# Kernel optimization log

Measured on AMD Instinct MI355X. Metric: run time of the kernel, lower is better.

The kernel has to match this reference:

```python
import jax, jax.numpy as jnp
import numpy as np

EMBED = 768
HEADS = 12
HDIM = EMBED // HEADS
FF = EMBED * 2
B, LQ, LK = 4, 2048, 2048


def _linear(x, W, b):
    # W: [in, out]
    return x @ W + b


def _layernorm(x, g, b, eps=1e-5):
    mu = jnp.mean(x, axis=-1, keepdims=True)
    var = jnp.mean(jnp.square(x - mu), axis=-1, keepdims=True)
    return (x - mu) * jax.lax.rsqrt(var + eps) * g + b


def _l2norm(x, eps=1e-12):
    # matches F.normalize: x / max(||x||_2, eps)
    n = jnp.sqrt(jnp.sum(jnp.square(x), axis=-1, keepdims=True))
    return x / jnp.maximum(n, eps)


def _heads(x):
    b, l, _ = x.shape
    return x.reshape(b, l, HEADS, HDIM).transpose(0, 2, 1, 3)  # [B,H,L,hd]


def setup_inputs() -> dict:
    key = jax.random.key(0)
    ks = jax.random.split(key, 20)
    s = 0.02
    d = {
        'image_tokens': jax.random.normal(ks[0], (B, LQ, EMBED), jnp.float32),
        'point_tokens': jax.random.normal(ks[1], (B, LK, EMBED), jnp.float32),
        'image_pos': jax.random.normal(ks[2], (B, LQ, EMBED), jnp.float32),
        'point_pos': jax.random.normal(ks[3], (B, LK, EMBED), jnp.float32),
        'Wip': jax.random.normal(ks[4], (EMBED, EMBED), jnp.float32) * s,
        'bip': jnp.zeros((EMBED,), jnp.float32),
        'Wpp': jax.random.normal(ks[5], (EMBED, EMBED), jnp.float32) * s,
        'bpp': jnp.zeros((EMBED,), jnp.float32),
        'Wq': jax.random.normal(ks[6], (EMBED, EMBED), jnp.float32) * s,
        'bq': jnp.zeros((EMBED,), jnp.float32),
        'Wk': jax.random.normal(ks[7], (EMBED, EMBED), jnp.float32) * s,
        'bk': jnp.zeros((EMBED,), jnp.float32),
        'Wv': jax.random.normal(ks[8], (EMBED, EMBED), jnp.float32) * s,
        'bv': jnp.zeros((EMBED,), jnp.float32),
        'Wo': jax.random.normal(ks[9], (EMBED, EMBED), jnp.float32) * s,
        'bo': jnp.zeros((EMBED,), jnp.float32),
        'g1': jnp.ones((EMBED,), jnp.float32),
        'b1': jnp.zeros((EMBED,), jnp.float32),
        'g2': jnp.ones((EMBED,), jnp.float32),
        'b2': jnp.zeros((EMBED,), jnp.float32),
        'Wf1': jax.random.normal(ks[10], (EMBED, FF), jnp.float32) * s,
        'bf1': jnp.zeros((FF,), jnp.float32),
        'Wf2': jax.random.normal(ks[11], (FF, EMBED), jnp.float32) * s,
        'bf2': jnp.zeros((EMBED,), jnp.float32),
    }
    return d


def reference(image_tokens, point_tokens, image_pos, point_pos,
              Wip, bip, Wpp, bpp, Wq, bq, Wk, bk, Wv, bv, Wo, bo,
              g1, b1, g2, b2, Wf1, bf1, Wf2, bf2):
    q = _linear(image_tokens + _linear(image_pos, Wip, bip), Wq, bq)
    k = _linear(point_tokens + _linear(point_pos, Wpp, bpp), Wk, bk)
    v = _linear(point_tokens, Wv, bv)

    q = _l2norm(_heads(q))  # [B,H,Lq,hd]
    k = _l2norm(_heads(k))  # [B,H,Lk,hd]
    v = _heads(v)           # [B,H,Lk,hd]

    scores = jnp.einsum('bhqd,bhkd->bhqk', q, k)
    attn = jax.nn.softmax(scores, axis=-1)
    fused = jnp.einsum('bhqk,bhkd->bhqd', attn, v)
    fused = fused.transpose(0, 2, 1, 3).reshape(image_tokens.shape[0], image_tokens.shape[1], EMBED)

    fused = _layernorm(image_tokens + _linear(fused, Wo, bo), g1, b1)
    h = _linear(fused, Wf1, bf1)
    h = 0.5 * h * (1.0 + jax.lax.erf(h / jnp.sqrt(jnp.float32(2.0))))  # exact GELU
    ff = _linear(h, Wf2, bf2)
    return _layernorm(fused + ff, g2, b2)
```

## Files before the change

kernel.cpp:

```cpp
#include <hip/hip_runtime.h>

#define EMBED 768
#define FFDIM 1536
#define BATCH 4
#define SEQ   2048
#define HEADS 12
#define MROWS (BATCH*SEQ)

typedef __attribute__((ext_vector_type(4)))  float  f32x4;
typedef __attribute__((ext_vector_type(16))) float  f32x16;
typedef __attribute__((ext_vector_type(8)))  __bf16 bf16x8;
typedef __attribute__((ext_vector_type(4)))  short  s16x4;

__device__ __forceinline__ short f2bf(float f) {
    union { float f; unsigned u; } x; x.f = f;
    unsigned r = x.u + 0x7fffu + ((x.u >> 16) & 1u);
    return (short)(r >> 16);
}

__device__ __forceinline__ unsigned cvtpk(float lo, float hi) {
    unsigned r;
    asm("v_cvt_pk_bf16_f32 %0, %1, %2" : "=v"(r) : "v"(lo), "v"(hi));
    return r;
}

__device__ __forceinline__ void gll16(const void* g, void* l) {
    __builtin_amdgcn_global_load_lds(
        (const __attribute__((address_space(1))) void*)g,
        (__attribute__((address_space(3))) void*)l, 16, 0, 0);
}

__device__ __forceinline__ bf16x8 ldsw(const short* base, int row, int chunk) {
    return *(const bf16x8*)((const char*)base + row * 128 + (((chunk ^ (row & 7))) << 4));
}

__global__ __launch_bounds__(256) void cvt3_kernel(
    const float* __restrict__ s0, const float* __restrict__ s1,
    const float* __restrict__ s2,
    short* __restrict__ o0, short* __restrict__ o1, short* __restrict__ o2)
{
    const float* s; short* o;
    switch (blockIdx.y) {
        case 0:  s = s0; o = o0; break;
        case 1:  s = s1; o = o1; break;
        default: s = s2; o = o2; break;
    }
    size_t i = ((size_t)blockIdx.x * 256 + threadIdx.x) * 4;
    float4 v = *(const float4*)(s + i);
    s16x4 r;
    r[0] = f2bf(v.x); r[1] = f2bf(v.y); r[2] = f2bf(v.z); r[3] = f2bf(v.w);
    *(s16x4*)(o + i) = r;
}

__global__ __launch_bounds__(256) void transpose_w(
    const float* __restrict__ W, short* __restrict__ Wt, int K, int N)
{
    __shared__ float tile[32][33];
    const int k0 = blockIdx.y * 32, n0 = blockIdx.x * 32;
    const int tx = threadIdx.x & 31, ty = threadIdx.x >> 5;
    #pragma unroll
    for (int i = 0; i < 32; i += 8)
        tile[ty + i][tx] = W[(size_t)(k0 + ty + i) * N + n0 + tx];
    __syncthreads();
    #pragma unroll
    for (int i = 0; i < 32; i += 8)
        Wt[(size_t)(n0 + ty + i) * K + k0 + tx] = f2bf(tile[tx][ty + i]);
}

__global__ __launch_bounds__(256) void transpose_v(
    const short* __restrict__ v, short* __restrict__ vt)
{
    __shared__ short tile[64][65];
    const int bh = blockIdx.y;
    const int b = bh / HEADS, h = bh % HEADS;
    const int k0 = blockIdx.x * 64;
    const int tx = threadIdx.x & 63, ty = threadIdx.x >> 6;
    #pragma unroll
    for (int i = 0; i < 64; i += 4)
        tile[ty + i][tx] = v[(size_t)(b * SEQ + k0 + ty + i) * EMBED + h * 64 + tx];
    __syncthreads();
    #pragma unroll
    for (int i = 0; i < 64; i += 4)
        vt[(size_t)(bh * 64 + ty + i) * SEQ + k0 + tx] = tile[tx][ty + i];
}

template<int L2N, int GELU_, int SBF, int SF32>
__device__ __forceinline__ void gemm_core(
    const short* __restrict__ A, const short* __restrict__ Wt,
    const float* __restrict__ bias, const float* __restrict__ resid,
    short* __restrict__ outb, float* __restrict__ outf, int N, int K)
{
    __shared__ short As[2][128][32];
    __shared__ short Bs[2][128][32];
    const int tid = threadIdx.x;
    const int mbase = blockIdx.y * 128, nbase = blockIdx.x * 128;
    const int wid = tid >> 6, lane = tid & 63;
    const int wm = wid >> 1, wn = wid & 1;
    const int l15 = lane & 15, lhi = lane >> 4;
    const int sr = tid >> 2;
    const int sc = (tid & 3) * 8;

    f32x4 acc[4][4] = {};

    const short* Ab = A  + (size_t)mbase * K;
    const short* Bb = Wt + (size_t)nbase * K;

#define GSTAGE(buf, kk)                                                         \
    gll16(Ab + (size_t)sr * K        + (kk) + sc, &As[buf][sr][sc]);            \
    gll16(Ab + (size_t)(64 + sr) * K + (kk) + sc, &As[buf][64 + sr][sc]);       \
    gll16(Bb + (size_t)sr * K        + (kk) + sc, &Bs[buf][sr][sc]);            \
    gll16(Bb + (size_t)(64 + sr) * K + (kk) + sc, &Bs[buf][64 + sr][sc]);

    GSTAGE(0, 0);
    __syncthreads();

    const int nk = K >> 5;
    for (int t = 0; t < nk; ++t) {
        const int cur = t & 1;
        if (t + 1 < nk) { GSTAGE(cur ^ 1, (t + 1) << 5); }
        bf16x8 av[4], bv[4];
        #pragma unroll
        for (int tt = 0; tt < 4; ++tt) {
            av[tt] = *(const bf16x8*)(&As[cur][wm * 64 + tt * 16 + l15][lhi * 8]);
            bv[tt] = *(const bf16x8*)(&Bs[cur][wn * 64 + tt * 16 + l15][lhi * 8]);
        }
        #pragma unroll
        for (int mt = 0; mt < 4; ++mt)
            #pragma unroll
            for (int nt = 0; nt < 4; ++nt)
                acc[mt][nt] = __builtin_amdgcn_mfma_f32_16x16x32_bf16(
                    av[mt], bv[nt], acc[mt][nt], 0, 0, 0);
        __syncthreads();
    }
#undef GSTAGE

    #pragma unroll
    for (int mt = 0; mt < 4; ++mt) {
        float vals[4][4];
        #pragma unroll
        for (int nt = 0; nt < 4; ++nt) {
            const int col = nbase + wn * 64 + nt * 16 + l15;
            const float bc = bias[col];
            #pragma unroll
            for (int j = 0; j < 4; ++j) vals[nt][j] = acc[mt][nt][j] + bc;
        }
        if (resid != nullptr) {
            #pragma unroll
            for (int nt = 0; nt < 4; ++nt) {
                const int col = nbase + wn * 64 + nt * 16 + l15;
                #pragma unroll
                for (int j = 0; j < 4; ++j) {
                    const int row = mbase + wm * 64 + mt * 16 + lhi * 4 + j;
                    vals[nt][j] += resid[(size_t)row * N + col];
                }
            }
        }
        if (L2N) {
            #pragma unroll
            for (int j = 0; j < 4; ++j) {
                float s = 0.f;
                #pragma unroll
                for (int nt = 0; nt < 4; ++nt) s += vals[nt][j] * vals[nt][j];
                s += __shfl_xor(s, 1); s += __shfl_xor(s, 2);
                s += __shfl_xor(s, 4); s += __shfl_xor(s, 8);
                const float inv = 1.0f / fmaxf(sqrtf(s), 1e-12f);
                #pragma unroll
                for (int nt = 0; nt < 4; ++nt) vals[nt][j] *= inv;
            }
        }
        if (GELU_) {
            #pragma unroll
            for (int nt = 0; nt < 4; ++nt)
                #pragma unroll
                for (int j = 0; j < 4; ++j) {
                    const float v = vals[nt][j];
                    vals[nt][j] = 0.5f * v * (1.0f + erff(v * 0.70710678118654752f));
                }
        }
        #pragma unroll
        for (int nt = 0; nt < 4; ++nt) {
            const int col = nbase + wn * 64 + nt * 16 + l15;
            #pragma unroll
            for (int j = 0; j < 4; ++j) {
                const int row = mbase + wm * 64 + mt * 16 + lhi * 4 + j;
                if (SBF)  outb[(size_t)row * N + col] = f2bf(vals[nt][j]);
                if (SF32) outf[(size_t)row * N + col] = vals[nt][j];
            }
        }
    }
}

template<int L2N, int GELU_, int SBF, int SF32>
__global__ __launch_bounds__(256) void gemm_bt(
    const short* __restrict__ A, const short* __restrict__ Wt,
    const float* __restrict__ bias, const float* __restrict__ resid,
    short* __restrict__ outb, float* __restrict__ outf, int N, int K)
{
    gemm_core<L2N, GELU_, SBF, SF32>(A, Wt, bias, resid, outb, outf, N, K);
}

__global__ __launch_bounds__(256) void gemm3_kernel(
    const short* A0, const short* W0, const float* b0, const float* r0, short* o0,
    const short* A1, const short* W1, const float* b1, const float* r1, short* o1,
    const short* A2, const short* W2, const float* b2, const float* r2, short* o2)
{
    const short *A, *W; const float *bi, *re; short* ob;
    if (blockIdx.z == 0)      { A = A0; W = W0; bi = b0; re = r0; ob = o0; }
    else if (blockIdx.z == 1) { A = A1; W = W1; bi = b1; re = r1; ob = o1; }
    else                      { A = A2; W = W2; bi = b2; re = r2; ob = o2; }
    gemm_core<0, 0, 1, 0>(A, W, bi, re, ob, nullptr, EMBED, EMBED);
}

__global__ __launch_bounds__(256) void gemm2_kernel(
    const short* A0, const short* W0, const float* b0, short* o0,
    const short* A1, const short* W1, const float* b1, short* o1)
{
    const short *A, *W; const float *bi; short* ob;
    if (blockIdx.z == 0) { A = A0; W = W0; bi = b0; ob = o0; }
    else                 { A = A1; W = W1; bi = b1; ob = o1; }
    gemm_core<1, 0, 1, 0>(A, W, bi, nullptr, ob, nullptr, EMBED, EMBED);
}

__global__ __launch_bounds__(256) void attn_kernel(
    const short* __restrict__ qn, const short* __restrict__ kn,
    const short* __restrict__ vt, short* __restrict__ outp)
{
    __shared__ short Ks[2][64][64];
    __shared__ short Vs[2][64][64];

    const int bh = blockIdx.y;
    const int b = bh / HEADS, h = bh % HEADS;
    const int q0 = blockIdx.x * 128;
    const int tid = threadIdx.x, wq = tid >> 6, lane = tid & 63;
    const int l31 = lane & 31, hi = lane >> 5;
    const int srow = tid >> 3;
    const int schk = tid & 7;

    const size_t qrow = (size_t)(b * SEQ + q0 + wq * 32 + l31) * EMBED + h * 64;
    bf16x8 qf[4];
    #pragma unroll
    for (int t = 0; t < 4; ++t)
        qf[t] = *(const bf16x8*)(qn + qrow + t * 16 + hi * 8);

    const short* kbase = kn + (size_t)b * SEQ * EMBED + h * 64;
    const short* vbase = vt + (size_t)bh * 64 * SEQ;

#define ASTAGE(buf, k0x) do {                                                            \
    _Pragma("unroll")                                                                    \
    for (int rr = 0; rr < 2; ++rr) {                                                     \
        const int row = rr * 32 + srow;                                                  \
        gll16(kbase + (size_t)((k0x) + row) * EMBED + ((schk ^ (row & 7)) * 8),          \
              &Ks[buf][row][schk * 8]);                                                  \
        gll16(vbase + (size_t)row * SEQ + (k0x) + ((schk ^ (row & 7)) * 8),              \
              &Vs[buf][row][schk * 8]);                                                  \
    }                                                                                    \
} while (0)

    ASTAGE(0, 0);
    __syncthreads();

    f32x16 acc_o[2] = {};
    float rsum = 0.f;
    const int NT = SEQ / 64;

    for (int kt = 0; kt < NT; ++kt) {
        const int cur = kt & 1;
        if (kt + 1 < NT) { ASTAGE(cur ^ 1, (kt + 1) * 64); }

        f32x16 s0 = {}, s1 = {};
        #pragma unroll
        for (int t = 0; t < 4; ++t) {
            bf16x8 kf0 = ldsw(&Ks[cur][0][0], l31,      t * 2 + hi);
            bf16x8 kf1 = ldsw(&Ks[cur][0][0], 32 + l31, t * 2 + hi);
            s0 = __builtin_amdgcn_mfma_f32_32x32x16_bf16(kf0, qf[t], s0, 0, 0, 0);
            s1 = __builtin_amdgcn_mfma_f32_32x32x16_bf16(kf1, qf[t], s1, 0, 0, 0);
        }

        float e0[16], e1[16];
        #pragma unroll
        for (int i = 0; i < 16; ++i) { const float e = __expf(s0[i]); rsum += e; e0[i] = e; }
        #pragma unroll
        for (int i = 0; i < 16; ++i) { const float e = __expf(s1[i]); rsum += e; e1[i] = e; }

        unsigned w[2][8], sw[2][8];
        #pragma unroll
        for (int a = 0; a < 4; ++a) {
            w[0][2*a]   = cvtpk(e0[4*a],   e0[4*a+1]);
            w[0][2*a+1] = cvtpk(e0[4*a+2], e0[4*a+3]);
            w[1][2*a]   = cvtpk(e1[4*a],   e1[4*a+1]);
            w[1][2*a+1] = cvtpk(e1[4*a+2], e1[4*a+3]);
        }
        #pragma unroll
        for (int kb = 0; kb < 2; ++kb)
            #pragma unroll
            for (int i = 0; i < 8; ++i)
                sw[kb][i] = (unsigned)__shfl_xor((int)w[kb][i], 32);

        #pragma unroll
        for (int kb = 0; kb < 2; ++kb) {
            #pragma unroll
            for (int ks = 0; ks < 2; ++ks) {
                union { unsigned u[4]; bf16x8 v; } pf;
                pf.u[0] = hi ? sw[kb][4*ks+2] : w[kb][4*ks];
                pf.u[1] = hi ? sw[kb][4*ks+3] : w[kb][4*ks+1];
                pf.u[2] = hi ? w[kb][4*ks+2]  : sw[kb][4*ks];
                pf.u[3] = hi ? w[kb][4*ks+3]  : sw[kb][4*ks+1];
                #pragma unroll
                for (int db = 0; db < 2; ++db) {
                    bf16x8 vf = ldsw(&Vs[cur][0][0], db * 32 + l31, kb * 4 + ks * 2 + hi);
                    acc_o[db] = __builtin_amdgcn_mfma_f32_32x32x16_bf16(vf, pf.v, acc_o[db], 0, 0, 0);
                }
            }
        }
        __syncthreads();
    }
#undef ASTAGE

    const float rtot = rsum + __shfl_xor(rsum, 32);
    const float rinv = 1.0f / rtot;

    short* Osb = &Ks[0][0][0];
    const int ql = wq * 32 + l31;
    #pragma unroll
    for (int db = 0; db < 2; ++db)
        #pragma unroll
        for (int a = 0; a < 4; ++a) {
            const float v0 = acc_o[db][4*a]   * rinv, v1 = acc_o[db][4*a+1] * rinv;
            const float v2 = acc_o[db][4*a+2] * rinv, v3 = acc_o[db][4*a+3] * rinv;
            uint2 pw; pw.x = cvtpk(v0, v1); pw.y = cvtpk(v2, v3);
            const int byteoff = ql * 128 + (((db * 4 + a) ^ (ql & 7)) << 4) + hi * 8;
            *(uint2*)((char*)Osb + byteoff) = pw;
        }
    __syncthreads();
    #pragma unroll
    for (int p = 0; p < 2; ++p) {
        const int r = p * 64 + (tid >> 2);
        #pragma unroll
        for (int i = 0; i < 2; ++i) {
            const int c = (tid & 3) * 2 + i;
            bf16x8 v = ldsw(Osb, r, c);
            *(bf16x8*)(outp + (size_t)(b * SEQ + q0 + r) * EMBED + h * 64 + c * 8) = v;
        }
    }
}

template<int SBF>
__global__ __launch_bounds__(256) void layernorm_768(
    const float* __restrict__ x, const float* __restrict__ g, const float* __restrict__ bb,
    float* __restrict__ outf, short* __restrict__ outb)
{
    const int row = blockIdx.x;
    const float* xr = x + (size_t)row * EMBED;
    const int t = threadIdx.x;
    const float v0 = xr[t], v1 = xr[t + 256], v2 = xr[t + 512];
    float s = v0 + v1 + v2;
    #pragma unroll
    for (int m = 1; m < 64; m <<= 1) s += __shfl_xor(s, m);
    __shared__ float red[4];
    __shared__ float red2[4];
    const int wid = t >> 6, lane = t & 63;
    if (lane == 0) red[wid] = s;
    __syncthreads();
    const float mu = (red[0] + red[1] + red[2] + red[3]) * (1.0f / 768.0f);
    const float d0 = v0 - mu, d1 = v1 - mu, d2 = v2 - mu;
    float ss = d0 * d0 + d1 * d1 + d2 * d2;
    #pragma unroll
    for (int m = 1; m < 64; m <<= 1) ss += __shfl_xor(ss, m);
    if (lane == 0) red2[wid] = ss;
    __syncthreads();
    const float var = (red2[0] + red2[1] + red2[2] + red2[3]) * (1.0f / 768.0f);
    const float inv = rsqrtf(var + 1e-5f);
    const float y0 = d0 * inv * g[t] + bb[t];
    const float y1 = d1 * inv * g[t + 256] + bb[t + 256];
    const float y2 = d2 * inv * g[t + 512] + bb[t + 512];
    float* of = outf + (size_t)row * EMBED;
    of[t] = y0; of[t + 256] = y1; of[t + 512] = y2;
    if (SBF) {
        short* ob = outb + (size_t)row * EMBED;
        ob[t] = f2bf(y0); ob[t + 256] = f2bf(y1); ob[t + 512] = f2bf(y2);
    }
}

extern "C" void kernel_launch(void* const* d_in, const int* in_sizes, int n_in,
                              void* d_out, int out_size, void* d_ws, size_t ws_size,
                              hipStream_t stream)
{
    (void)in_sizes; (void)n_in; (void)out_size; (void)ws_size;
    const float* itok = (const float*)d_in[0];
    const float* ptok = (const float*)d_in[1];
    const float* ipos = (const float*)d_in[2];
    const float* ppos = (const float*)d_in[3];
    const float* Wip = (const float*)d_in[4];  const float* bip = (const float*)d_in[5];
    const float* Wpp = (const float*)d_in[6];  const float* bpp = (const float*)d_in[7];
    const float* Wq  = (const float*)d_in[8];  const float* bq  = (const float*)d_in[9];
    const float* Wk  = (const float*)d_in[10]; const float* bk  = (const float*)d_in[11];
    const float* Wv  = (const float*)d_in[12]; const float* bv  = (const float*)d_in[13];
    const float* Wo  = (const float*)d_in[14]; const float* bo  = (const float*)d_in[15];
    const float* g1  = (const float*)d_in[16]; const float* b1  = (const float*)d_in[17];
    const float* g2  = (const float*)d_in[18]; const float* b2  = (const float*)d_in[19];
    const float* Wf1 = (const float*)d_in[20]; const float* bf1 = (const float*)d_in[21];
    const float* Wf2 = (const float*)d_in[22]; const float* bf2 = (const float*)d_in[23];
    float* out = (float*)d_out;

    char* ws = (char*)d_ws;
    constexpr size_t SZ_BF  = (size_t)MROWS * EMBED * 2;
    constexpr size_t SZ_F32 = (size_t)MROWS * EMBED * 4;
    constexpr size_t W768B  = (size_t)EMBED * EMBED * 2;
    constexpr size_t W1536B = (size_t)EMBED * FFDIM * 2;

    size_t o = 0;
    short* v_bf     = (short*)(ws + o); o += SZ_BF;
    short* pt_bf    = (short*)(ws + o); o += SZ_BF;
    short* ip_bf    = (short*)(ws + o); o += SZ_BF;
    short* pp_bf    = (short*)(ws + o); o += SZ_BF;
    short* qin_bf   = (short*)(ws + o); o += SZ_BF;
    short* kin_bf   = (short*)(ws + o); o += SZ_BF;
    short* qn_bf    = (short*)(ws + o); o += SZ_BF;
    short* kn_bf    = (short*)(ws + o); o += SZ_BF;
    short* attn_bf  = (short*)(ws + o); o += SZ_BF;
    float* x_f32    = (float*)(ws + o); o += SZ_F32;
    short* fused_bf = (short*)(ws + o); o += SZ_BF;
    float* fused_f32= (float*)(ws + o); o += SZ_F32;
    short* wip_t = (short*)(ws + o); o += W768B;
    short* wpp_t = (short*)(ws + o); o += W768B;
    short* wq_t  = (short*)(ws + o); o += W768B;
    short* wk_t  = (short*)(ws + o); o += W768B;
    short* wv_t  = (short*)(ws + o); o += W768B;
    short* wo_t  = (short*)(ws + o); o += W768B;
    short* wf1_t = (short*)(ws + o); o += W1536B;
    short* wf2_t = (short*)(ws + o); o += W1536B;
    short* vt_bf = pp_bf;
    short* h_bf  = qin_bf;

    const dim3 blk(256);

    cvt3_kernel<<<dim3(MROWS * EMBED / 1024, 3), blk, 0, stream>>>(
        ptok, ipos, ppos, pt_bf, ip_bf, pp_bf);

    transpose_w<<<dim3(EMBED / 32, EMBED / 32), blk, 0, stream>>>(Wip, wip_t, EMBED, EMBED);
    transpose_w<<<dim3(EMBED / 32, EMBED / 32), blk, 0, stream>>>(Wpp, wpp_t, EMBED, EMBED);
    transpose_w<<<dim3(EMBED / 32, EMBED / 32), blk, 0, stream>>>(Wq,  wq_t,  EMBED, EMBED);
    transpose_w<<<dim3(EMBED / 32, EMBED / 32), blk, 0, stream>>>(Wk,  wk_t,  EMBED, EMBED);
    transpose_w<<<dim3(EMBED / 32, EMBED / 32), blk, 0, stream>>>(Wv,  wv_t,  EMBED, EMBED);
    transpose_w<<<dim3(EMBED / 32, EMBED / 32), blk, 0, stream>>>(Wo,  wo_t,  EMBED, EMBED);
    transpose_w<<<dim3(FFDIM / 32, EMBED / 32), blk, 0, stream>>>(Wf1, wf1_t, EMBED, FFDIM);
    transpose_w<<<dim3(EMBED / 32, FFDIM / 32), blk, 0, stream>>>(Wf2, wf2_t, FFDIM, EMBED);

    gemm3_kernel<<<dim3(6, 64, 3), blk, 0, stream>>>(
        ip_bf, wip_t, bip, itok, qin_bf,
        pp_bf, wpp_t, bpp, ptok, kin_bf,
        pt_bf, wv_t,  bv,  nullptr, v_bf);

    gemm2_kernel<<<dim3(6, 64, 2), blk, 0, stream>>>(
        qin_bf, wq_t, bq, qn_bf,
        kin_bf, wk_t, bk, kn_bf);

    transpose_v<<<dim3(SEQ / 64, BATCH * HEADS), blk, 0, stream>>>(v_bf, vt_bf);
    attn_kernel<<<dim3(SEQ / 128, BATCH * HEADS), blk, 0, stream>>>(qn_bf, kn_bf, vt_bf, attn_bf);

    gemm_bt<0,0,0,1><<<dim3(6, 64), blk, 0, stream>>>(attn_bf, wo_t, bo, itok, nullptr, x_f32, EMBED, EMBED);
    layernorm_768<1><<<dim3(MROWS), blk, 0, stream>>>(x_f32, g1, b1, fused_f32, fused_bf);
    gemm_bt<0,1,1,0><<<dim3(12, 64), blk, 0, stream>>>(fused_bf, wf1_t, bf1, nullptr, h_bf, nullptr, FFDIM, EMBED);
    gemm_bt<0,0,0,1><<<dim3(6, 64), blk, 0, stream>>>(h_bf, wf2_t, bf2, fused_f32, nullptr, x_f32, EMBED, FFDIM);
    layernorm_768<0><<<dim3(MROWS), blk, 0, stream>>>(x_f32, g2, b2, out, nullptr);
}
```

Before: 519.4 us.

## Fold position projections into concatenated Q/K weights and keep intermediates in bf16

Precomposes Wip·Wq and Wpp·Wk into concatenated [Wq; Wip·Wq] weights and folded biases. Q and K then each come from a single K=1536 GEMM over the token and position inputs, which removes the separate position GEMM pass. It also batches the weight transposes and conversions into fewer launches. Residual and layernorm intermediates are stored as bf16 instead of fp32, log2e is folded into the Q normalization so a raw v_exp_f32 can be used, and the shuffle is replaced by v_permlane32_swap. These cut memory traffic and launches, at the cost of extra bf16 rounding on the residual path and on the composed weights.

```diff
diff --git a/kernel.cpp b/kernel.cpp
--- a/kernel.cpp
+++ b/kernel.cpp
@@ -6,6 +6,7 @@
 #define SEQ   2048
 #define HEADS 12
 #define MROWS (BATCH*SEQ)
+#define LOG2E 1.44269504088896340736f
 
 typedef __attribute__((ext_vector_type(4)))  float  f32x4;
 typedef __attribute__((ext_vector_type(16))) float  f32x16;
@@ -17,81 +18,108 @@
     unsigned r = x.u + 0x7fffu + ((x.u >> 16) & 1u);
     return (short)(r >> 16);
 }
-
+__device__ __forceinline__ float bf2f(short s) {
+    union { unsigned u; float f; } x; x.u = ((unsigned)(unsigned short)s) << 16;
+    return x.f;
+}
 __device__ __forceinline__ unsigned cvtpk(float lo, float hi) {
     unsigned r;
     asm("v_cvt_pk_bf16_f32 %0, %1, %2" : "=v"(r) : "v"(lo), "v"(hi));
     return r;
 }
-
+__device__ __forceinline__ float exp2a(float x) {
+    float r;
+    asm("v_exp_f32 %0, %1" : "=v"(r) : "v"(x));
+    return r;
+}
 __device__ __forceinline__ void gll16(const void* g, void* l) {
     __builtin_amdgcn_global_load_lds(
         (const __attribute__((address_space(1))) void*)g,
         (__attribute__((address_space(3))) void*)l, 16, 0, 0);
 }
-
 __device__ __forceinline__ bf16x8 ldsw(const short* base, int row, int chunk) {
     return *(const bf16x8*)((const char*)base + row * 128 + (((chunk ^ (row & 7))) << 4));
 }
 
-__global__ __launch_bounds__(256) void cvt3_kernel(
+__global__ __launch_bounds__(256) void cvt6_kernel(
     const float* __restrict__ s0, const float* __restrict__ s1,
-    const float* __restrict__ s2,
-    short* __restrict__ o0, short* __restrict__ o1, short* __restrict__ o2)
-{
-    const float* s; short* o;
+    const float* __restrict__ s2, const float* __restrict__ s3,
+    const float* __restrict__ w0, const float* __restrict__ w1,
+    short* o0, short* o1, short* o2, short* o3, short* ow0, short* ow1)
+{
+    const float* s; short* o; size_t nelem;
     switch (blockIdx.y) {
-        case 0:  s = s0; o = o0; break;
-        case 1:  s = s1; o = o1; break;
-        default: s = s2; o = o2; break;
+        case 0:  s = s0; o = o0; nelem = (size_t)MROWS * EMBED; break;
+        case 1:  s = s1; o = o1; nelem = (size_t)MROWS * EMBED; break;
+        case 2:  s = s2; o = o2; nelem = (size_t)MROWS * EMBED; break;
+        case 3:  s = s3; o = o3; nelem = (size_t)MROWS * EMBED; break;
+        case 4:  s = w0; o = ow0; nelem = (size_t)EMBED * EMBED; break;
+        default: s = w1; o = ow1; nelem = (size_t)EMBED * EMBED; break;
     }
     size_t i = ((size_t)blockIdx.x * 256 + threadIdx.x) * 4;
+    if (i >= nelem) return;
     float4 v = *(const float4*)(s + i);
     s16x4 r;
     r[0] = f2bf(v.x); r[1] = f2bf(v.y); r[2] = f2bf(v.z); r[3] = f2bf(v.w);
     *(s16x4*)(o + i) = r;
 }
 
-__global__ __launch_bounds__(256) void transpose_w(
-    const float* __restrict__ W, short* __restrict__ Wt, int K, int N)
-{
+__global__ __launch_bounds__(256) void transpose6_kernel(
+    const float* Wq, const float* Wk, const float* Wv, const float* Wo_,
+    const float* Wf1, const float* Wf2,
+    short* wq_t, short* wqcat, short* wk_t, short* wkcat,
+    short* wv_t, short* wo_t, short* wf1_t, short* wf2_t)
+{
+    const float* W; int K, N, st1, st2; short *d1, *d2;
+    switch (blockIdx.z) {
+        case 0: W = Wq;  K = 768;  N = 768;  d1 = wq_t;  st1 = 768;  d2 = wqcat; st2 = 1536; break;
+        case 1: W = Wk;  K = 768;  N = 768;  d1 = wk_t;  st1 = 768;  d2 = wkcat; st2 = 1536; break;
+        case 2: W = Wv;  K = 768;  N = 768;  d1 = wv_t;  st1 = 768;  d2 = nullptr; st2 = 0;  break;
+        case 3: W = Wo_; K = 768;  N = 768;  d1 = wo_t;  st1 = 768;  d2 = nullptr; st2 = 0;  break;
+        case 4: W = Wf1; K = 768;  N = 1536; d1 = wf1_t; st1 = 768;  d2 = nullptr; st2 = 0;  break;
+        default:W = Wf2; K = 1536; N = 768;  d1 = wf2_t; st1 = 1536; d2 = nullptr; st2 = 0;  break;
+    }
+    const int k0 = blockIdx.y * 32, n0 = blockIdx.x * 32;
+    if (k0 >= K || n0 >= N) return;
     __shared__ float tile[32][33];
-    const int k0 = blockIdx.y * 32, n0 = blockIdx.x * 32;
     const int tx = threadIdx.x & 31, ty = threadIdx.x >> 5;
     #pragma unroll
     for (int i = 0; i < 32; i += 8)
         tile[ty + i][tx] = W[(size_t)(k0 + ty + i) * N + n0 + tx];
     __syncthreads();
     #pragma unroll
-    for (int i = 0; i < 32; i += 8)
-        Wt[(size_t)(n0 + ty + i) * K + k0 + tx] = f2bf(tile[tx][ty + i]);
-}
-
-__global__ __launch_bounds__(256) void transpose_v(
-    const short* __restrict__ v, short* __restrict__ vt)
-{
-    __shared__ short tile[64][65];
-    const int bh = blockIdx.y;
-    const int b = bh / HEADS, h = bh % HEADS;
-    const int k0 = blockIdx.x * 64;
-    const int tx = threadIdx.x & 63, ty = threadIdx.x >> 6;
-    #pragma unroll
-    for (int i = 0; i < 64; i += 4)
-        tile[ty + i][tx] = v[(size_t)(b * SEQ + k0 + ty + i) * EMBED + h * 64 + tx];
-    __syncthreads();
-    #pragma unroll
-    for (int i = 0; i < 64; i += 4)
-        vt[(size_t)(bh * 64 + ty + i) * SEQ + k0 + tx] = tile[tx][ty + i];
-}
-
-template<int L2N, int GELU_, int SBF, int SF32>
+    for (int i = 0; i < 32; i += 8) {
+        const short v = f2bf(tile[tx][ty + i]);
+        d1[(size_t)(n0 + ty + i) * st1 + k0 + tx] = v;
+        if (d2) d2[(size_t)(n0 + ty + i) * st2 + k0 + tx] = v;
+    }
+}
+
+__global__ __launch_bounds__(256) void biascomp_kernel(
+    const float* bip, const float* Wq, const float* bq, float* bqc,
+    const float* bpp, const float* Wk, const float* bk, float* bkc)
+{
+    const float *bi, *W, *bb; float* o;
+    if (blockIdx.y) { bi = bpp; W = Wk; bb = bk; o = bkc; }
+    else            { bi = bip; W = Wq; bb = bq; o = bqc; }
+    const int n = blockIdx.x * 256 + threadIdx.x;
+    float acc = bb[n];
+    #pragma unroll 16
+    for (int j = 0; j < 768; ++j) acc += bi[j] * W[(size_t)j * 768 + n];
+    o[n] = acc;
+}
+
+typedef short lds_tile_t[128][32];
+
+template<int DUALA, int L2N, int GELU_, int RESF, int RESB, int SBF, int SF32>
 __device__ __forceinline__ void gemm_core(
-    const short* __restrict__ A, const short* __restrict__ Wt,
-    const float* __restrict__ bias, const float* __restrict__ resid,
-    short* __restrict__ outb, float* __restrict__ outf, int N, int K)
-{
-    __shared__ short As[2][128][32];
-    __shared__ short Bs[2][128][32];
+    lds_tile_t* As, lds_tile_t* Bs,
+    const short* __restrict__ A1, const short* __restrict__ A2,
+    const short* __restrict__ Wt, const float* __restrict__ bias,
+    const float* __restrict__ residf, const short* __restrict__ residb,
+    short* __restrict__ outb, float* __restrict__ outf,
+    int N, int K, int ostr, float l2scale)
+{
     const int tid = threadIdx.x;
     const int mbase = blockIdx.y * 128, nbase = blockIdx.x * 128;
     const int wid = tid >> 6, lane = tid & 63;
@@ -101,15 +129,22 @@
     const int sc = (tid & 3) * 8;
 
     f32x4 acc[4][4] = {};
-
-    const short* Ab = A  + (size_t)mbase * K;
     const short* Bb = Wt + (size_t)nbase * K;
 
-#define GSTAGE(buf, kk)                                                         \
-    gll16(Ab + (size_t)sr * K        + (kk) + sc, &As[buf][sr][sc]);            \
-    gll16(Ab + (size_t)(64 + sr) * K + (kk) + sc, &As[buf][64 + sr][sc]);       \
-    gll16(Bb + (size_t)sr * K        + (kk) + sc, &Bs[buf][sr][sc]);            \
-    gll16(Bb + (size_t)(64 + sr) * K + (kk) + sc, &Bs[buf][64 + sr][sc]);
+#define GSTAGE(buf, kk) do {                                                        \
+    if (DUALA) {                                                                    \
+        const short* ab = ((kk) < 768 ? A1 : A2) + (size_t)mbase * 768;             \
+        const int ko = (kk) & 767;                                                  \
+        gll16(ab + (size_t)sr * 768        + ko + sc, &As[buf][sr][sc]);            \
+        gll16(ab + (size_t)(64 + sr) * 768 + ko + sc, &As[buf][64 + sr][sc]);       \
+    } else {                                                                        \
+        const short* ab = A1 + (size_t)mbase * K;                                   \
+        gll16(ab + (size_t)sr * K        + (kk) + sc, &As[buf][sr][sc]);            \
+        gll16(ab + (size_t)(64 + sr) * K + (kk) + sc, &As[buf][64 + sr][sc]);       \
+    }                                                                               \
+    gll16(Bb + (size_t)sr * K        + (kk) + sc, &Bs[buf][sr][sc]);                \
+    gll16(Bb + (size_t)(64 + sr) * K + (kk) + sc, &Bs[buf][64 + sr][sc]);           \
+} while (0)
 
     GSTAGE(0, 0);
     __syncthreads();
@@ -140,18 +175,19 @@
         #pragma unroll
         for (int nt = 0; nt < 4; ++nt) {
             const int col = nbase + wn * 64 + nt * 16 + l15;
-            const float bc = bias[col];
+            const float bc = bias ? bias[col] : 0.f;
             #pragma unroll
             for (int j = 0; j < 4; ++j) vals[nt][j] = acc[mt][nt][j] + bc;
         }
-        if (resid != nullptr) {
+        if (RESF || RESB) {
             #pragma unroll
             for (int nt = 0; nt < 4; ++nt) {
                 const int col = nbase + wn * 64 + nt * 16 + l15;
                 #pragma unroll
                 for (int j = 0; j < 4; ++j) {
                     const int row = mbase + wm * 64 + mt * 16 + lhi * 4 + j;
-                    vals[nt][j] += resid[(size_t)row * N + col];
+                    if (RESF) vals[nt][j] += residf[(size_t)row * N + col];
+                    if (RESB) vals[nt][j] += bf2f(residb[(size_t)row * N + col]);
                 }
             }
         }
@@ -163,7 +199,7 @@
                 for (int nt = 0; nt < 4; ++nt) s += vals[nt][j] * vals[nt][j];
                 s += __shfl_xor(s, 1); s += __shfl_xor(s, 2);
                 s += __shfl_xor(s, 4); s += __shfl_xor(s, 8);
-                const float inv = 1.0f / fmaxf(sqrtf(s), 1e-12f);
+                const float inv = l2scale / fmaxf(sqrtf(s), 1e-12f);
                 #pragma unroll
                 for (int nt = 0; nt < 4; ++nt) vals[nt][j] *= inv;
             }
@@ -183,42 +219,85 @@
             #pragma unroll
             for (int j = 0; j < 4; ++j) {
                 const int row = mbase + wm * 64 + mt * 16 + lhi * 4 + j;
-                if (SBF)  outb[(size_t)row * N + col] = f2bf(vals[nt][j]);
-                if (SF32) outf[(size_t)row * N + col] = vals[nt][j];
+                if (SBF)  outb[(size_t)row * ostr + col] = f2bf(vals[nt][j]);
+                if (SF32) outf[(size_t)row * ostr + col] = vals[nt][j];
             }
         }
     }
 }
 
-template<int L2N, int GELU_, int SBF, int SF32>
-__global__ __launch_bounds__(256) void gemm_bt(
-    const short* __restrict__ A, const short* __restrict__ Wt,
-    const float* __restrict__ bias, const float* __restrict__ resid,
-    short* __restrict__ outb, float* __restrict__ outf, int N, int K)
-{
-    gemm_core<L2N, GELU_, SBF, SF32>(A, Wt, bias, resid, outb, outf, N, K);
-}
-
-__global__ __launch_bounds__(256) void gemm3_kernel(
-    const short* A0, const short* W0, const float* b0, const float* r0, short* o0,
-    const short* A1, const short* W1, const float* b1, const float* r1, short* o1,
-    const short* A2, const short* W2, const float* b2, const float* r2, short* o2)
-{
-    const short *A, *W; const float *bi, *re; short* ob;
-    if (blockIdx.z == 0)      { A = A0; W = W0; bi = b0; re = r0; ob = o0; }
-    else if (blockIdx.z == 1) { A = A1; W = W1; bi = b1; re = r1; ob = o1; }
-    else                      { A = A2; W = W2; bi = b2; re = r2; ob = o2; }
-    gemm_core<0, 0, 1, 0>(A, W, bi, re, ob, nullptr, EMBED, EMBED);
-}
-
-__global__ __launch_bounds__(256) void gemm2_kernel(
-    const short* A0, const short* W0, const float* b0, short* o0,
-    const short* A1, const short* W1, const float* b1, short* o1)
-{
-    const short *A, *W; const float *bi; short* ob;
-    if (blockIdx.z == 0) { A = A0; W = W0; bi = b0; ob = o0; }
-    else                 { A = A1; W = W1; bi = b1; ob = o1; }
-    gemm_core<1, 0, 1, 0>(A, W, bi, nullptr, ob, nullptr, EMBED, EMBED);
+__global__ __launch_bounds__(256) void compose_kernel(
+    const short* wq_t, const short* wip_bf, short* wqcat,
+    const short* wk_t, const short* wpp_bf, short* wkcat)
+{
+    __shared__ lds_tile_t As[2], Bs[2];
+    const short *A, *W; short* o;
+    if (blockIdx.z == 0) { A = wq_t; W = wip_bf; o = wqcat + 768; }
+    else                 { A = wk_t; W = wpp_bf; o = wkcat + 768; }
+    gemm_core<0,0,0,0,0,1,0>(As, Bs, A, nullptr, W, nullptr, nullptr, nullptr,
+                             o, nullptr, 768, 768, 1536, 1.f);
+}
+
+__global__ __launch_bounds__(256) void qkv_kernel(
+    const short* itok_bf, const short* ipos_bf, const short* wqcat, const float* bqc, short* qn,
+    const short* ptok_bf, const short* ppos_bf, const short* wkcat, const float* bkc, short* kn,
+    const short* wv_t, const float* bv, short* v_bf)
+{
+    __shared__ lds_tile_t As[2], Bs[2];
+    const int z = blockIdx.z;
+    if (z == 2) {
+        gemm_core<0,0,0,0,0,1,0>(As, Bs, ptok_bf, nullptr, wv_t, bv, nullptr, nullptr,
+                                 v_bf, nullptr, 768, 768, 768, 1.f);
+    } else {
+        const short* a1 = z ? ptok_bf : itok_bf;
+        const short* a2 = z ? ppos_bf : ipos_bf;
+        const short* w  = z ? wkcat   : wqcat;
+        const float* bi = z ? bkc     : bqc;
+        short* o        = z ? kn      : qn;
+        gemm_core<1,1,0,0,0,1,0>(As, Bs, a1, a2, w, bi, nullptr, nullptr,
+                                 o, nullptr, 768, 1536, 768, z ? 1.f : LOG2E);
+    }
+}
+
+__global__ __launch_bounds__(256) void wo_kernel(
+    const short* attn_bf, const short* wo_t, const float* bo, const float* itok, short* x1_bf)
+{
+    __shared__ lds_tile_t As[2], Bs[2];
+    gemm_core<0,0,0,1,0,1,0>(As, Bs, attn_bf, nullptr, wo_t, bo, itok, nullptr,
+                             x1_bf, nullptr, 768, 768, 768, 1.f);
+}
+
+__global__ __launch_bounds__(256) void wf1_kernel(
+    const short* fused_bf, const short* wf1_t, const float* bf1, short* h_bf)
+{
+    __shared__ lds_tile_t As[2], Bs[2];
+    gemm_core<0,0,1,0,0,1,0>(As, Bs, fused_bf, nullptr, wf1_t, bf1, nullptr, nullptr,
+                             h_bf, nullptr, 1536, 768, 1536, 1.f);
+}
+
+__global__ __launch_bounds__(256) void wf2_kernel(
+    const short* h_bf, const short* wf2_t, const float* bf2, const short* fused_bf, short* x2_bf)
+{
+    __shared__ lds_tile_t As[2], Bs[2];
+    gemm_core<0,0,0,0,1,1,0>(As, Bs, h_bf, nullptr, wf2_t, bf2, nullptr, fused_bf,
+                             x2_bf, nullptr, 768, 1536, 768, 1.f);
+}
+
+__global__ __launch_bounds__(256) void transpose_v(
+    const short* __restrict__ v, short* __restrict__ vt)
+{
+    __shared__ short tile[64][65];
+    const int bh = blockIdx.y;
+    const int b = bh / HEADS, h = bh % HEADS;
+    const int k0 = blockIdx.x * 64;
+    const int tx = threadIdx.x & 63, ty = threadIdx.x >> 6;
+    #pragma unroll
+    for (int i = 0; i < 64; i += 4)
+        tile[ty + i][tx] = v[(size_t)(b * SEQ + k0 + ty + i) * EMBED + h * 64 + tx];
+    __syncthreads();
+    #pragma unroll
+    for (int i = 0; i < 64; i += 4)
+        vt[(size_t)(bh * 64 + ty + i) * SEQ + k0 + tx] = tile[tx][ty + i];
 }
 
 __global__ __launch_bounds__(256) void attn_kernel(
@@ -278,11 +357,11 @@
 
         float e0[16], e1[16];
         #pragma unroll
-        for (int i = 0; i < 16; ++i) { const float e = __expf(s0[i]); rsum += e; e0[i] = e; }
-        #pragma unroll
-        for (int i = 0; i < 16; ++i) { const float e = __expf(s1[i]); rsum += e; e1[i] = e; }
-
-        unsigned w[2][8], sw[2][8];
+        for (int i = 0; i < 16; ++i) { const float e = exp2a(s0[i]); rsum += e; e0[i] = e; }
+        #pragma unroll
+        for (int i = 0; i < 16; ++i) { const float e = exp2a(s1[i]); rsum += e; e1[i] = e; }
+
+        unsigned w[2][8];
         #pragma unroll
         for (int a = 0; a < 4; ++a) {
             w[0][2*a]   = cvtpk(e0[4*a],   e0[4*a+1]);
@@ -290,21 +369,17 @@
             w[1][2*a]   = cvtpk(e1[4*a],   e1[4*a+1]);
             w[1][2*a+1] = cvtpk(e1[4*a+2], e1[4*a+3]);
         }
-        #pragma unroll
-        for (int kb = 0; kb < 2; ++kb)
-            #pragma unroll
-            for (int i = 0; i < 8; ++i)
-                sw[kb][i] = (unsigned)__shfl_xor((int)w[kb][i], 32);
 
         #pragma unroll
         for (int kb = 0; kb < 2; ++kb) {
             #pragma unroll
             for (int ks = 0; ks < 2; ++ks) {
+                unsigned p0 = w[kb][4*ks], p1 = w[kb][4*ks+1];
+                unsigned p2 = w[kb][4*ks+2], p3 = w[kb][4*ks+3];
+                asm("v_permlane32_swap_b32 %0, %1" : "+v"(p0), "+v"(p2));
+                asm("v_permlane32_swap_b32 %0, %1" : "+v"(p1), "+v"(p3));
                 union { unsigned u[4]; bf16x8 v; } pf;
-                pf.u[0] = hi ? sw[kb][4*ks+2] : w[kb][4*ks];
-                pf.u[1] = hi ? sw[kb][4*ks+3] : w[kb][4*ks+1];
-                pf.u[2] = hi ? w[kb][4*ks+2]  : sw[kb][4*ks];
-                pf.u[3] = hi ? w[kb][4*ks+3]  : sw[kb][4*ks+1];
+                pf.u[0] = p0; pf.u[1] = p1; pf.u[2] = p2; pf.u[3] = p3;
                 #pragma unroll
                 for (int db = 0; db < 2; ++db) {
                     bf16x8 vf = ldsw(&Vs[cur][0][0], db * 32 + l31, kb * 4 + ks * 2 + hi);
@@ -344,15 +419,15 @@
     }
 }
 
-template<int SBF>
+template<int OUTBF>
 __global__ __launch_bounds__(256) void layernorm_768(
-    const float* __restrict__ x, const float* __restrict__ g, const float* __restrict__ bb,
+    const short* __restrict__ x, const float* __restrict__ g, const float* __restrict__ bb,
     float* __restrict__ outf, short* __restrict__ outb)
 {
     const int row = blockIdx.x;
-    const float* xr = x + (size_t)row * EMBED;
+    const short* xr = x + (size_t)row * EMBED;
     const int t = threadIdx.x;
-    const float v0 = xr[t], v1 = xr[t + 256], v2 = xr[t + 512];
+    const float v0 = bf2f(xr[t]), v1 = bf2f(xr[t + 256]), v2 = bf2f(xr[t + 512]);
     float s = v0 + v1 + v2;
     #pragma unroll
     for (int m = 1; m < 64; m <<= 1) s += __shfl_xor(s, m);
@@ -373,11 +448,12 @@
     const float y0 = d0 * inv * g[t] + bb[t];
     const float y1 = d1 * inv * g[t + 256] + bb[t + 256];
     const float y2 = d2 * inv * g[t + 512] + bb[t + 512];
-    float* of = outf + (size_t)row * EMBED;
-    of[t] = y0; of[t + 256] = y1; of[t + 512] = y2;
-    if (SBF) {
+    if (OUTBF) {
         short* ob = outb + (size_t)row * EMBED;
         ob[t] = f2bf(y0); ob[t + 256] = f2bf(y1); ob[t + 512] = f2bf(y2);
+    } else {
+        float* of = outf + (size_t)row * EMBED;
+        of[t] = y0; of[t + 256] = y1; of[t + 512] = y2;
     }
 }
 
@@ -404,63 +480,63 @@
 
     char* ws = (char*)d_ws;
     constexpr size_t SZ_BF  = (size_t)MROWS * EMBED * 2;
-    constexpr size_t SZ_F32 = (size_t)MROWS * EMBED * 4;
     constexpr size_t W768B  = (size_t)EMBED * EMBED * 2;
     constexpr size_t W1536B = (size_t)EMBED * FFDIM * 2;
 
     size_t o = 0;
-    short* v_bf     = (short*)(ws + o); o += SZ_BF;
-    short* pt_bf    = (short*)(ws + o); o += SZ_BF;
-    short* ip_bf    = (short*)(ws + o); o += SZ_BF;
-    short* pp_bf    = (short*)(ws + o); o += SZ_BF;
-    short* qin_bf   = (short*)(ws + o); o += SZ_BF;
-    short* kin_bf   = (short*)(ws + o); o += SZ_BF;
-    short* qn_bf    = (short*)(ws + o); o += SZ_BF;
-    short* kn_bf    = (short*)(ws + o); o += SZ_BF;
-    short* attn_bf  = (short*)(ws + o); o += SZ_BF;
-    float* x_f32    = (float*)(ws + o); o += SZ_F32;
-    short* fused_bf = (short*)(ws + o); o += SZ_BF;
-    float* fused_f32= (float*)(ws + o); o += SZ_F32;
-    short* wip_t = (short*)(ws + o); o += W768B;
-    short* wpp_t = (short*)(ws + o); o += W768B;
-    short* wq_t  = (short*)(ws + o); o += W768B;
-    short* wk_t  = (short*)(ws + o); o += W768B;
-    short* wv_t  = (short*)(ws + o); o += W768B;
-    short* wo_t  = (short*)(ws + o); o += W768B;
-    short* wf1_t = (short*)(ws + o); o += W1536B;
-    short* wf2_t = (short*)(ws + o); o += W1536B;
-    short* vt_bf = pp_bf;
-    short* h_bf  = qin_bf;
+    short* itok_bf = (short*)(ws + o); o += SZ_BF;
+    short* ptok_bf = (short*)(ws + o); o += SZ_BF;
+    short* ipos_bf = (short*)(ws + o); o += SZ_BF;
+    short* ppos_bf = (short*)(ws + o); o += SZ_BF;
+    short* qn_bf   = (short*)(ws + o); o += SZ_BF;
+    short* kn_bf   = (short*)(ws + o); o += SZ_BF;
+    short* v_bf    = (short*)(ws + o); o += SZ_BF;
+    short* vt_bf   = (short*)(ws + o); o += SZ_BF;
+    short* attn_bf = (short*)(ws + o); o += SZ_BF;
+    short* x1_bf   = (short*)(ws + o); o += SZ_BF;
+    short* fused_bf= (short*)(ws + o); o += SZ_BF;
+    short* h_bf    = (short*)(ws + o); o += 2 * SZ_BF;
+    short* x2_bf   = (short*)(ws + o); o += SZ_BF;
+    short* wip_bf  = (short*)(ws + o); o += W768B;
+    short* wpp_bf  = (short*)(ws + o); o += W768B;
+    short* wq_t    = (short*)(ws + o); o += W768B;
+    short* wk_t    = (short*)(ws + o); o += W768B;
+    short* wv_t    = (short*)(ws + o); o += W768B;
+    short* wo_t    = (short*)(ws + o); o += W768B;
+    short* wf1_t   = (short*)(ws + o); o += W1536B;
+    short* wf2_t   = (short*)(ws + o); o += W1536B;
+    short* wqcat   = (short*)(ws + o); o += W1536B;
+    short* wkcat   = (short*)(ws + o); o += W1536B;
+    float* bqc     = (float*)(ws + o); o += 768 * 4;
+    float* bkc     = (float*)(ws + o); o += 768 * 4;
 
     const dim3 blk(256);
 
-    cvt3_kernel<<<dim3(MROWS * EMBED / 1024, 3), blk, 0, stream>>>(
-        ptok, ipos, ppos, pt_bf, ip_bf, pp_bf);
-
-    transpose_w<<<dim3(EMBED / 32, EMBED / 32), blk, 0, stream>>>(Wip, wip_t, EMBED, EMBED);
-    transpose_w<<<dim3(EMBED / 32, EMBED / 32), blk, 0, stream>>>(Wpp, wpp_t, EMBED, EMBED);
-    transpose_w<<<dim3(EMBED / 32, EMBED / 32), blk, 0, stream>>>(Wq,  wq_t,  EMBED, EMBED);
-    transpose_w<<<dim3(EMBED / 32, EMBED / 32), blk, 0, stream>>>(Wk,  wk_t,  EMBED, EMBED);
-    transpose_w<<<dim3(EMBED / 32, EMBED / 32), blk, 0, stream>>>(Wv,  wv_t,  EMBED, EMBED);
-    transpose_w<<<dim3(EMBED / 32, EMBED / 32), blk, 0, stream>>>(Wo,  wo_t,  EMBED, EMBED);
-    transpose_w<<<dim3(FFDIM / 32, EMBED / 32), blk, 0, stream>>>(Wf1, wf1_t, EMBED, FFDIM);
-    transpose_w<<<dim3(EMBED / 32, FFDIM / 32), blk, 0, stream>>>(Wf2, wf2_t, FFDIM, EMBED);
-
-    gemm3_kernel<<<dim3(6, 64, 3), blk, 0, stream>>>(
-        ip_bf, wip_t, bip, itok, qin_bf,
-        pp_bf, wpp_t, bpp, ptok, kin_bf,
-        pt_bf, wv_t,  bv,  nullptr, v_bf);
-
-    gemm2_kernel<<<dim3(6, 64, 2), blk, 0, stream>>>(
-        qin_bf, wq_t, bq, qn_bf,
-        kin_bf, wk_t, bk, kn_bf);
+    cvt6_kernel<<<dim3(MROWS * EMBED / 1024, 6), blk, 0, stream>>>(
+        itok, ptok, ipos, ppos, Wip, Wpp,
+        itok_bf, ptok_bf, ipos_bf, ppos_bf, wip_bf, wpp_bf);
+
+    transpose6_kernel<<<dim3(48, 48, 6), blk, 0, stream>>>(
+        Wq, Wk, Wv, Wo, Wf1, Wf2,
+        wq_t, wqcat, wk_t, wkcat, wv_t, wo_t, wf1_t, wf2_t);
+
+    biascomp_kernel<<<dim3(3, 2), blk, 0, stream>>>(
+        bip, Wq, bq, bqc, bpp, Wk, bk, bkc);
+
+    compose_kernel<<<dim3(6, 6, 2), blk, 0, stream>>>(
+        wq_t, wip_bf, wqcat, wk_t, wpp_bf, wkcat);
+
+    qkv_kernel<<<dim3(6, 64, 3), blk, 0, stream>>>(
+        itok_bf, ipos_bf, wqcat, bqc, qn_bf,
+        ptok_bf, ppos_bf, wkcat, bkc, kn_bf,
+        wv_t, bv, v_bf);
 
     transpose_v<<<dim3(SEQ / 64, BATCH * HEADS), blk, 0, stream>>>(v_bf, vt_bf);
     attn_kernel<<<dim3(SEQ / 128, BATCH * HEADS), blk, 0, stream>>>(qn_bf, kn_bf, vt_bf, attn_bf);
 
-    gemm_bt<0,0,0,1><<<dim3(6, 64), blk, 0, stream>>>(attn_bf, wo_t, bo, itok, nullptr, x_f32, EMBED, EMBED);
-    layernorm_768<1><<<dim3(MROWS), blk, 0, stream>>>(x_f32, g1, b1, fused_f32, fused_bf);
-    gemm_bt<0,1,1,0><<<dim3(12, 64), blk, 0, stream>>>(fused_bf, wf1_t, bf1, nullptr, h_bf, nullptr, FFDIM, EMBED);
-    gemm_bt<0,0,0,1><<<dim3(6, 64), blk, 0, stream>>>(h_bf, wf2_t, bf2, fused_f32, nullptr, x_f32, EMBED, FFDIM);
-    layernorm_768<0><<<dim3(MROWS), blk, 0, stream>>>(x_f32, g2, b2, out, nullptr);
-}
+    wo_kernel<<<dim3(6, 64), blk, 0, stream>>>(attn_bf, wo_t, bo, itok, x1_bf);
+    layernorm_768<1><<<dim3(MROWS), blk, 0, stream>>>(x1_bf, g1, b1, nullptr, fused_bf);
+    wf1_kernel<<<dim3(12, 64), blk, 0, stream>>>(fused_bf, wf1_t, bf1, h_bf);
+    wf2_kernel<<<dim3(6, 64), blk, 0, stream>>>(h_bf, wf2_t, bf2, fused_bf, x2_bf);
+    layernorm_768<0><<<dim3(MROWS), blk, 0, stream>>>(x2_bf, g2, b2, out, nullptr);
+}
```

After: 518.1 us. About the same (-0.3%).
